# Optimization experiments

Measured on AMD Instinct MI355X. Metric: run time of the kernel, lower is better.

## Reference

```python
import jax, jax.numpy as jnp
import numpy as np

NUM_CLASSES = 4
PROTO_MOMENTUM = 0.9
CONF_THRESH = 0.8
LAMBDA_INTRA = 1.0
LAMBDA_INTER = 0.1
MARGIN_M = 1.0


def setup_inputs() -> dict:
    key = jax.random.key(0)
    k1, k2, k3, k4 = jax.random.split(key, 4)
    B, C, H, W, D = 2, 64, 96, 96, 96
    K = NUM_CLASSES + 1
    feat = jax.random.normal(k1, (B, C, H, W, D), dtype=jnp.float32)
    # softmax predictions; sharpen logits so a realistic fraction exceeds conf_thresh
    logits = jax.random.normal(k2, (B, K, H, W, D), dtype=jnp.float32)
    pred = jax.nn.softmax(4.0 * logits, axis=1)
    label = jax.random.randint(k3, (B, 1, H, W, D), 0, K, dtype=jnp.int32)
    is_labelled = jnp.ones((B,), dtype=bool)
    prototypes = jax.random.normal(k4, (NUM_CLASSES, C), dtype=jnp.float32)
    return {"feat": feat, "pred": pred, "label": label,
            "is_labelled": is_labelled, "prototypes": prototypes}


def reference(feat, pred, label, is_labelled, prototypes):
    B, C, H, W, D = feat.shape
    K = pred.shape[1]
    N = B * H * W * D
    dt = feat.dtype

    # flatten spatial dims: (N, C), (N, K), (N,)
    feat_flat = jnp.transpose(feat, (0, 2, 3, 4, 1)).reshape(-1, C)
    pred_flat = jnp.transpose(pred, (0, 2, 3, 4, 1)).reshape(-1, K)
    label_flat = label.reshape(-1)
    is_lab_flat = jnp.broadcast_to(is_labelled[:, None], (B, H * W * D)).reshape(-1)

    # high-confidence mask
    pred_conf = jnp.max(pred_flat, axis=1)
    pred_class = jnp.argmax(pred_flat, axis=1).astype(jnp.int32)
    conf_mask = (pred_conf > CONF_THRESH) & (pred_class > 0)
    conf_mask = conf_mask & ((pred_class == label_flat) | ~is_lab_flat)

    # segmented per-class mean over masked voxels (single scatter-add pass)
    seg = jnp.where(conf_mask, pred_class - 1, NUM_CLASSES)  # dummy bucket for masked-out
    maskf = conf_mask.astype(dt)
    cnt = jax.ops.segment_sum(maskf, seg, num_segments=NUM_CLASSES + 1)[:NUM_CLASSES]
    sums = jax.ops.segment_sum(feat_flat * maskf[:, None], seg,
                               num_segments=NUM_CLASSES + 1)[:NUM_CLASSES]
    class_mean = sums / jnp.maximum(cnt, 1.0)[:, None]
    present = cnt > 0

    # EMA prototype update (buffer update: no grad through the batch means)
    proto_new = jnp.where(
        present[:, None],
        PROTO_MOMENTUM * prototypes + (1.0 - PROTO_MOMENTUM) * jax.lax.stop_gradient(class_mean),
        prototypes,
    )

    # intra-class compactness: mean over masked voxels of ||f_i - mu_{c_i}||^2
    proto_per_vox = proto_new[jnp.clip(pred_class - 1, 0, NUM_CLASSES - 1)]  # (N, C)
    d2 = jnp.sum((feat_flat - proto_per_vox) ** 2, axis=1)
    n_valid = jnp.sum(maskf)
    loss_intra = jnp.sum(maskf * d2) / jnp.maximum(n_valid, 1.0)

    # inter-class separation: hinge on pairwise prototype distances (upper triangle)
    diff = proto_new[:, None, :] - proto_new[None, :, :]
    dist = jnp.sqrt(jnp.sum(diff ** 2, axis=2) + 1e-12)
    triu = jnp.triu(jnp.ones((NUM_CLASSES, NUM_CLASSES), dtype=bool), k=1)
    viol = jnp.maximum(MARGIN_M - dist, 0.0) ** 2
    n_pairs = NUM_CLASSES * (NUM_CLASSES - 1) // 2
    loss_inter = jnp.sum(jnp.where(triu, viol, 0.0)) / n_pairs

    loss_total = LAMBDA_INTRA * loss_intra + LAMBDA_INTER * loss_inter
    return loss_total, loss_intra, loss_inter, proto_new
```

## Files before the change

kernel.cpp:

```cpp
#include <hip/hip_runtime.h>

#define HWD 884736
#define KCLS 5
#define CCH 64
#define NC 4

constexpr int PLANE4 = HWD / 4;
constexpr int GRP_B  = HWD / 4;
constexpr int NBLK   = 2 * GRP_B / 256;
constexpr int NPART  = 16;
constexpr int PARTSZ = 272;
constexpr int MASK_OFF_BYTES = 32768;

__global__ __launch_bounds__(256) void pm_zero(float* __restrict__ part) {
    const int n = NPART * PARTSZ;
    for (int i = threadIdx.x; i < n; i += 256) part[i] = 0.f;
}

__global__ __launch_bounds__(256) void pm_mask(
    const float* __restrict__ pred, const int* __restrict__ label,
    const unsigned char* __restrict__ is_lab,
    unsigned int* __restrict__ mask, float* __restrict__ part)
{
    __shared__ float lcnt[NC];
    const int t = threadIdx.x;
    if (t < NC) lcnt[t] = 0.f;
    __syncthreads();

    const int g = blockIdx.x * 256 + t;
    const int b = (blockIdx.x >= NBLK / 2);
    const int gg = g - b * GRP_B;

    const float4* pb = (const float4*)(pred + (size_t)b * KCLS * HWD) + gg;
    float4 pk[KCLS];
    #pragma unroll
    for (int k = 0; k < KCLS; ++k) pk[k] = pb[(size_t)k * PLANE4];
    const int4 lb = ((const int4*)(label + (size_t)b * HWD))[gg];
    const bool lab = is_lab[b] != 0;

    unsigned int wd = 0;
    #pragma unroll
    for (int j = 0; j < 4; ++j) {
        float best = -1.f; int bi = 0;
        #pragma unroll
        for (int k = 0; k < KCLS; ++k) {
            float v = ((const float*)&pk[k])[j];
            if (v > best) { best = v; bi = k; }
        }
        const int lj = ((const int*)&lb)[j];
        const bool m = (best > 0.8f) & (bi > 0) & ((bi == lj) | (!lab));
        if (m) {
            wd |= (4u | (unsigned)(bi - 1)) << (3 * j);
            atomicAdd(&lcnt[bi - 1], 1.f);
        }
    }
    mask[g] = wd;
    __syncthreads();
    if (t < NC) {
        float c = lcnt[t];
        if (c != 0.f) atomicAdd(&part[(size_t)(blockIdx.x & (NPART - 1)) * PARTSZ + 256 + t], c);
    }
}

__global__ __launch_bounds__(256, 2) void pm_dense(
    const float* __restrict__ feat, const unsigned int* __restrict__ mask,
    float* __restrict__ part)
{
    __shared__ float4 red[64 * 65];
    const int t = threadIdx.x, w = t >> 6, l = t & 63;
    const int bi = blockIdx.x;
    const int b = (bi >= NBLK / 2);
    const int g0 = bi * 256 - b * GRP_B;
    const float4* fb = (const float4*)feat + (size_t)b * CCH * PLANE4;
    const int c0 = w * 16;

    float4 acc[16];
    #pragma unroll
    for (int u = 0; u < 16; ++u) acc[u] = make_float4(0.f, 0.f, 0.f, 0.f);
    float sq[NC] = {0.f, 0.f, 0.f, 0.f};

    for (int i = 0; i < 4; ++i) {
        const int gl = i * 64 + l;
        const int gg = g0 + gl;
        const unsigned int wm = mask[bi * 256 + gl];

        float4 fv[16];
        #pragma unroll
        for (int u = 0; u < 16; ++u)
            fv[u] = fb[(size_t)(c0 + u) * PLANE4 + gg];

        float ind[4][NC];
        #pragma unroll
        for (int j = 0; j < 4; ++j) {
            const int bits = (wm >> (3 * j)) & 7;
            #pragma unroll
            for (int k = 0; k < NC; ++k)
                ind[j][k] = (bits == (4 | k)) ? 1.f : 0.f;
        }

        float vsq[4] = {0.f, 0.f, 0.f, 0.f};
        #pragma unroll
        for (int u = 0; u < 16; ++u) {
            #pragma unroll
            for (int j = 0; j < 4; ++j) {
                const float v = ((const float*)&fv[u])[j];
                vsq[j] = fmaf(v, v, vsq[j]);
                #pragma unroll
                for (int k = 0; k < NC; ++k)
                    ((float*)&acc[u])[k] = fmaf(ind[j][k], v, ((float*)&acc[u])[k]);
            }
        }
        #pragma unroll
        for (int j = 0; j < 4; ++j)
            #pragma unroll
            for (int k = 0; k < NC; ++k)
                sq[k] = fmaf(ind[j][k], vsq[j], sq[k]);
    }

    #pragma unroll
    for (int u = 0; u < 16; ++u) red[(c0 + u) * 65 + l] = acc[u];

    #pragma unroll
    for (int k = 0; k < NC; ++k) {
        float v = sq[k];
        #pragma unroll
        for (int o = 1; o < 64; o <<= 1) v += __shfl_xor(v, o);
        sq[k] = v;
    }
    float* dst = part + (size_t)(bi & (NPART - 1)) * PARTSZ;
    if (l < NC) {
        float v = (l == 0) ? sq[0] : (l == 1) ? sq[1] : (l == 2) ? sq[2] : sq[3];
        if (v != 0.f) atomicAdd(&dst[260 + l], v);
    }
    __syncthreads();

    const int c = t >> 2, k = t & 3;
    float s = 0.f;
    #pragma unroll 8
    for (int l2 = 0; l2 < 64; ++l2) s += ((const float*)&red[c * 65 + l2])[k];
    if (s != 0.f) atomicAdd(&dst[k * 64 + c], s);
}

__global__ __launch_bounds__(256) void pm_pass2(
    const float* __restrict__ part, const float* __restrict__ proto,
    float* __restrict__ out)
{
    __shared__ float scnt[NC], ssq[NC], smu[NC * CCH], sred[4];
    __shared__ float s_intra;
    const int t = threadIdx.x;
    const int q = t >> 6;

    float s = 0.f;
    #pragma unroll
    for (int p = 0; p < NPART; ++p) s += part[p * PARTSZ + t];
    if (t < 2 * NC) {
        float a = 0.f;
        #pragma unroll
        for (int p = 0; p < NPART; ++p) a += part[p * PARTSZ + 256 + t];
        if (t < NC) scnt[t] = a; else ssq[t - NC] = a;
    }
    __syncthreads();

    const float cq = scnt[q];
    const float mean = s / fmaxf(cq, 1.f);
    const float pold = proto[t];
    const float mu = (cq > 0.f) ? 0.9f * pold + 0.1f * mean : pold;
    out[3 + t] = mu;
    smu[t] = mu;

    float pi = -2.f * s * mu + cq * mu * mu;
    #pragma unroll
    for (int o = 1; o < 64; o <<= 1) pi += __shfl_xor(pi, o);
    if ((t & 63) == 0) sred[t >> 6] = pi;
    __syncthreads();

    if (t == 0) {
        float num = sred[0] + sred[1] + sred[2] + sred[3]
                  + ssq[0] + ssq[1] + ssq[2] + ssq[3];
        float nv = scnt[0] + scnt[1] + scnt[2] + scnt[3];
        s_intra = num / fmaxf(nv, 1.f);
    }
    __syncthreads();

    if (t < 64) {
        const int pi_[6] = {0, 0, 0, 1, 1, 2};
        const int pj_[6] = {1, 2, 3, 2, 3, 3};
        float acc = 0.f;
        #pragma unroll
        for (int e = 0; e < 6; ++e) {
            float d = smu[pi_[e] * 64 + t] - smu[pj_[e] * 64 + t];
            float d2 = d * d;
            #pragma unroll
            for (int o = 1; o < 64; o <<= 1) d2 += __shfl_xor(d2, o);
            float dist = sqrtf(d2 + 1e-12f);
            float vv = fmaxf(1.f - dist, 0.f);
            acc += vv * vv;
        }
        if (t == 0) {
            float li = acc / 6.f;
            out[0] = s_intra + 0.1f * li;
            out[1] = s_intra;
            out[2] = li;
        }
    }
}

extern "C" void kernel_launch(void* const* d_in, const int* in_sizes, int n_in,
                              void* d_out, int out_size, void* d_ws, size_t ws_size,
                              hipStream_t stream) {
    const float* feat         = (const float*)d_in[0];
    const float* pred         = (const float*)d_in[1];
    const int* label          = (const int*)d_in[2];
    const unsigned char* ilab = (const unsigned char*)d_in[3];
    const float* proto        = (const float*)d_in[4];
    float* out                = (float*)d_out;
    float* part               = (float*)d_ws;
    unsigned int* mask        = (unsigned int*)((char*)d_ws + MASK_OFF_BYTES);

    hipLaunchKernelGGL(pm_zero,  dim3(1),    dim3(256), 0, stream, part);
    hipLaunchKernelGGL(pm_mask,  dim3(NBLK), dim3(256), 0, stream,
                       pred, label, ilab, mask, part);
    hipLaunchKernelGGL(pm_dense, dim3(NBLK), dim3(256), 0, stream, feat, mask, part);
    hipLaunchKernelGGL(pm_pass2, dim3(1),    dim3(256), 0, stream, part, proto, out);
}
```

Baseline: 110.1 us.

## Restructure feature reduction into per-channel plane sweeps with wave shuffles

Replaces the dense kernel, where each block read all 64 channels for 256 voxel groups and reduced through a large LDS tile, with a sweep kernel in which each block handles one (batch, channel, segment) tile of 27x256 float4s. Per-thread class sums and squared sums are kept in scalars, reduced with wave shuffles, and written with atomics, with no LDS and no __syncthreads. This aims to cut LDS use and register pressure, raise occupancy and make each block's access stream contiguous. The cost is that the mask is re-read once per channel (64 times) and many more atomics are issued, since every wave of every block now posts its own partials.

New measurement: 105.8 us. -3.9%, faster.

```diff
diff --git a/kernel.cpp b/kernel.cpp
--- a/kernel.cpp
+++ b/kernel.cpp
@@ -7,10 +7,15 @@
 
 constexpr int PLANE4 = HWD / 4;
 constexpr int GRP_B  = HWD / 4;
-constexpr int NBLK   = 2 * GRP_B / 256;
+constexpr int NBLKM  = 2 * GRP_B / 256;
 constexpr int NPART  = 16;
 constexpr int PARTSZ = 272;
 constexpr int MASK_OFF_BYTES = 32768;
+
+constexpr int ITER = 27;
+constexpr int SEGG = 256 * ITER;
+constexpr int NSEG = PLANE4 / SEGG;
+constexpr int NBLKS = 2 * CCH * NSEG;
 
 __global__ __launch_bounds__(256) void pm_zero(float* __restrict__ part) {
     const int n = NPART * PARTSZ;
@@ -28,7 +33,7 @@
     __syncthreads();
 
     const int g = blockIdx.x * 256 + t;
-    const int b = (blockIdx.x >= NBLK / 2);
+    const int b = (blockIdx.x >= NBLKM / 2);
     const int gg = g - b * GRP_B;
 
     const float4* pb = (const float4*)(pred + (size_t)b * KCLS * HWD) + gg;
@@ -41,104 +46,80 @@
     unsigned int wd = 0;
     #pragma unroll
     for (int j = 0; j < 4; ++j) {
-        float best = -1.f; int bi = 0;
+        float best = -1.f; int c = 0;
         #pragma unroll
         for (int k = 0; k < KCLS; ++k) {
             float v = ((const float*)&pk[k])[j];
-            if (v > best) { best = v; bi = k; }
+            if (v > best) { best = v; c = k; }
         }
         const int lj = ((const int*)&lb)[j];
-        const bool m = (best > 0.8f) & (bi > 0) & ((bi == lj) | (!lab));
+        const bool m = (best > 0.8f) & (c > 0) & ((c == lj) | (!lab));
         if (m) {
-            wd |= (4u | (unsigned)(bi - 1)) << (3 * j);
-            atomicAdd(&lcnt[bi - 1], 1.f);
+            wd |= (4u | (unsigned)(c - 1)) << (3 * j);
+            atomicAdd(&lcnt[c - 1], 1.f);
         }
     }
     mask[g] = wd;
     __syncthreads();
     if (t < NC) {
         float c = lcnt[t];
-        if (c != 0.f) atomicAdd(&part[(size_t)(blockIdx.x & (NPART - 1)) * PARTSZ + 256 + t], c);
-    }
-}
-
-__global__ __launch_bounds__(256, 2) void pm_dense(
+        if (c != 0.f)
+            atomicAdd(&part[(size_t)(blockIdx.x & (NPART - 1)) * PARTSZ + 256 + t], c);
+    }
+}
+
+__global__ __launch_bounds__(256) void pm_sweep(
     const float* __restrict__ feat, const unsigned int* __restrict__ mask,
     float* __restrict__ part)
 {
-    __shared__ float4 red[64 * 65];
-    const int t = threadIdx.x, w = t >> 6, l = t & 63;
+    const int t = threadIdx.x, l = t & 63;
     const int bi = blockIdx.x;
-    const int b = (bi >= NBLK / 2);
-    const int g0 = bi * 256 - b * GRP_B;
-    const float4* fb = (const float4*)feat + (size_t)b * CCH * PLANE4;
-    const int c0 = w * 16;
-
-    float4 acc[16];
-    #pragma unroll
-    for (int u = 0; u < 16; ++u) acc[u] = make_float4(0.f, 0.f, 0.f, 0.f);
-    float sq[NC] = {0.f, 0.f, 0.f, 0.f};
-
-    for (int i = 0; i < 4; ++i) {
-        const int gl = i * 64 + l;
-        const int gg = g0 + gl;
-        const unsigned int wm = mask[bi * 256 + gl];
-
-        float4 fv[16];
-        #pragma unroll
-        for (int u = 0; u < 16; ++u)
-            fv[u] = fb[(size_t)(c0 + u) * PLANE4 + gg];
-
-        float ind[4][NC];
+    const int b   = bi >> 11;
+    const int rem = bi & 2047;
+    const int c   = rem >> 5;
+    const int seg = rem & 31;
+    const int g0  = seg * SEGG;
+
+    const float4* fb = (const float4*)(feat + (size_t)(b * CCH + c) * HWD);
+    const unsigned int* mb = mask + (size_t)b * PLANE4;
+
+    float s0 = 0.f, s1 = 0.f, s2 = 0.f, s3 = 0.f;
+    float q0 = 0.f, q1 = 0.f, q2 = 0.f, q3 = 0.f;
+
+    #pragma unroll 3
+    for (int i = 0; i < ITER; ++i) {
+        const int gg = g0 + i * 256 + t;
+        const unsigned int wm = mb[gg];
+        const float4 f = fb[gg];
         #pragma unroll
         for (int j = 0; j < 4; ++j) {
             const int bits = (wm >> (3 * j)) & 7;
-            #pragma unroll
-            for (int k = 0; k < NC; ++k)
-                ind[j][k] = (bits == (4 | k)) ? 1.f : 0.f;
-        }
-
-        float vsq[4] = {0.f, 0.f, 0.f, 0.f};
-        #pragma unroll
-        for (int u = 0; u < 16; ++u) {
-            #pragma unroll
-            for (int j = 0; j < 4; ++j) {
-                const float v = ((const float*)&fv[u])[j];
-                vsq[j] = fmaf(v, v, vsq[j]);
-                #pragma unroll
-                for (int k = 0; k < NC; ++k)
-                    ((float*)&acc[u])[k] = fmaf(ind[j][k], v, ((float*)&acc[u])[k]);
-            }
-        }
-        #pragma unroll
-        for (int j = 0; j < 4; ++j)
-            #pragma unroll
-            for (int k = 0; k < NC; ++k)
-                sq[k] = fmaf(ind[j][k], vsq[j], sq[k]);
-    }
-
-    #pragma unroll
-    for (int u = 0; u < 16; ++u) red[(c0 + u) * 65 + l] = acc[u];
-
-    #pragma unroll
-    for (int k = 0; k < NC; ++k) {
-        float v = sq[k];
-        #pragma unroll
-        for (int o = 1; o < 64; o <<= 1) v += __shfl_xor(v, o);
-        sq[k] = v;
-    }
+            const float v = ((const float*)&f)[j];
+            const float v2 = v * v;
+            if (bits == 4) { s0 += v; q0 += v2; }
+            if (bits == 5) { s1 += v; q1 += v2; }
+            if (bits == 6) { s2 += v; q2 += v2; }
+            if (bits == 7) { s3 += v; q3 += v2; }
+        }
+    }
+
+    #pragma unroll
+    for (int o = 1; o < 64; o <<= 1) {
+        s0 += __shfl_xor(s0, o); s1 += __shfl_xor(s1, o);
+        s2 += __shfl_xor(s2, o); s3 += __shfl_xor(s3, o);
+        q0 += __shfl_xor(q0, o); q1 += __shfl_xor(q1, o);
+        q2 += __shfl_xor(q2, o); q3 += __shfl_xor(q3, o);
+    }
+
     float* dst = part + (size_t)(bi & (NPART - 1)) * PARTSZ;
     if (l < NC) {
-        float v = (l == 0) ? sq[0] : (l == 1) ? sq[1] : (l == 2) ? sq[2] : sq[3];
-        if (v != 0.f) atomicAdd(&dst[260 + l], v);
-    }
-    __syncthreads();
-
-    const int c = t >> 2, k = t & 3;
-    float s = 0.f;
-    #pragma unroll 8
-    for (int l2 = 0; l2 < 64; ++l2) s += ((const float*)&red[c * 65 + l2])[k];
-    if (s != 0.f) atomicAdd(&dst[k * 64 + c], s);
+        const float sv = (l == 0) ? s0 : (l == 1) ? s1 : (l == 2) ? s2 : s3;
+        if (sv != 0.f) atomicAdd(&dst[l * 64 + c], sv);
+    } else if (l < 2 * NC) {
+        const int k = l - NC;
+        const float qv = (k == 0) ? q0 : (k == 1) ? q1 : (k == 2) ? q2 : q3;
+        if (qv != 0.f) atomicAdd(&dst[260 + k], qv);
+    }
 }
 
 __global__ __launch_bounds__(256) void pm_pass2(
@@ -217,9 +198,9 @@
     float* part               = (float*)d_ws;
     unsigned int* mask        = (unsigned int*)((char*)d_ws + MASK_OFF_BYTES);
 
-    hipLaunchKernelGGL(pm_zero,  dim3(1),    dim3(256), 0, stream, part);
-    hipLaunchKernelGGL(pm_mask,  dim3(NBLK), dim3(256), 0, stream,
+    hipLaunchKernelGGL(pm_zero,  dim3(1),     dim3(256), 0, stream, part);
+    hipLaunchKernelGGL(pm_mask,  dim3(NBLKM), dim3(256), 0, stream,
                        pred, label, ilab, mask, part);
-    hipLaunchKernelGGL(pm_dense, dim3(NBLK), dim3(256), 0, stream, feat, mask, part);
-    hipLaunchKernelGGL(pm_pass2, dim3(1),    dim3(256), 0, stream, part, proto, out);
-}
+    hipLaunchKernelGGL(pm_sweep, dim3(NBLKS), dim3(256), 0, stream, feat, mask, part);
+    hipLaunchKernelGGL(pm_pass2, dim3(1),     dim3(256), 0, stream, part, proto, out);
+}
```
